# Kernel tuning notes

Measured on AMD Instinct MI355X. Metric: run time of the kernel, lower is better.

Reference implementation:

```python
import jax, jax.numpy as jnp
import numpy as np

B, N, H, NHEADS, N_COE, N_SCALES, THRE = 8, 1024, 128, 4, 50, 4, 5.0


def _layernorm(x, g, b, eps=1e-5):
    mu = x.mean(-1, keepdims=True)
    var = ((x - mu) ** 2).mean(-1, keepdims=True)
    return (x - mu) / jnp.sqrt(var + eps) * g + b


def setup_inputs() -> dict:
    key = jax.random.key(0)
    ks = jax.random.split(key, 12)

    def lin(k, out_d, in_d):
        lim = 1.0 / np.sqrt(in_d)
        kw, kb = jax.random.split(k)
        W = jax.random.uniform(kw, (out_d, in_d), minval=-lim, maxval=lim, dtype=jnp.float32)
        b = jax.random.uniform(kb, (out_d,), minval=-lim, maxval=lim, dtype=jnp.float32)
        return W, b

    eigw_W, eigw_b = lin(ks[0], H, H + 1)
    qkv_W, qkv_b = lin(ks[1], 3 * H, H)
    out_W, out_b = lin(ks[2], H, H)
    ffn1_W, ffn1_b = lin(ks[3], H, H)
    ffn2_W, ffn2_b = lin(ks[4], H, H)
    dsc_W, dsc_b = lin(ks[5], N_COE, H)
    dwav_W, dwav_b = lin(ks[6], N_COE, H)
    dscl_W, dscl_b = lin(ks[7], N_SCALES, H)
    # normalized-Laplacian eigenvalues live in [0, 2]
    eigenvalue = jax.random.uniform(ks[8], (B, N), minval=0.0, maxval=2.0, dtype=jnp.float32)
    eigenvector = jax.random.normal(ks[9], (B, N, N), dtype=jnp.float32) / np.sqrt(N)
    length = jnp.full((B,), N, dtype=jnp.int32)  # full graphs -> static shapes under jit
    return dict(
        eigenvalue=eigenvalue, eigenvector=eigenvector,
        eigw_W=eigw_W, eigw_b=eigw_b,
        ln1_g=jnp.ones((H,), jnp.float32), ln1_b=jnp.zeros((H,), jnp.float32),
        qkv_W=qkv_W, qkv_b=qkv_b, out_W=out_W, out_b=out_b,
        ln2_g=jnp.ones((H,), jnp.float32), ln2_b=jnp.zeros((H,), jnp.float32),
        ffn1_W=ffn1_W, ffn1_b=ffn1_b, ffn2_W=ffn2_W, ffn2_b=ffn2_b,
        dsc_W=dsc_W, dsc_b=dsc_b, dwav_W=dwav_W, dwav_b=dwav_b,
        dscl_W=dscl_W, dscl_b=dscl_b, length=length)


def _forward(eigenvalue, eigenvector, eigw_W, eigw_b, ln1_g, ln1_b, qkv_W, qkv_b,
             out_W, out_b, ln2_g, ln2_b, ffn1_W, ffn1_b, ffn2_W, ffn2_b,
             dsc_W, dsc_b, dwav_W, dwav_b, dscl_W, dscl_b, length):
    Bn, Nn = eigenvalue.shape
    mask1d = jnp.arange(Nn)[None, :] >= length[:, None]  # [B,N] True = padding

    # ---- SineEncoding ----
    ee = eigenvalue * 100.0
    div = jnp.exp(jnp.arange(0, H, 2, dtype=jnp.float32) * (-np.log(10000.0) / H))
    pe = ee[:, :, None] * div  # [B,N,H/2]
    eeig = jnp.concatenate([eigenvalue[:, :, None], jnp.sin(pe), jnp.cos(pe)], -1)  # [B,N,H+1]
    eig = eeig @ eigw_W.T + eigw_b  # [B,N,H]

    # ---- MHA block (pre-norm, residual) ----
    x = _layernorm(eig, ln1_g, ln1_b)
    qkv = x @ qkv_W.T + qkv_b
    q, k, v = jnp.split(qkv, 3, axis=-1)
    dh = H // NHEADS
    heads = lambda t: t.reshape(Bn, Nn, NHEADS, dh).transpose(0, 2, 1, 3)
    q, k, v = heads(q), heads(k), heads(v)
    scores = jnp.einsum('bhnd,bhmd->bhnm', q, k) / np.sqrt(dh)
    scores = jnp.where(mask1d[:, None, None, :], -1e9, scores)
    attn = jax.nn.softmax(scores, axis=-1)
    o = jnp.einsum('bhnm,bhmd->bhnd', attn, v).transpose(0, 2, 1, 3).reshape(Bn, Nn, H)
    eig = eig + (o @ out_W.T + out_b)

    # ---- FFN block (pre-norm, residual) ----
    y = _layernorm(eig, ln2_g, ln2_b)
    y = jax.nn.gelu(y @ ffn1_W.T + ffn1_b, approximate=False) @ ffn2_W.T + ffn2_b
    eig = eig + y

    # ---- decoders: masked mean-pool over eigenvalue axis ----
    len_f = length.astype(eig.dtype)[:, None] + 1e-8

    def pooled(W, b):
        c = eig @ W.T + b
        c = jnp.where(mask1d[:, :, None], 0.0, c)
        return c.sum(1) / len_f

    coe_scaling = jax.nn.sigmoid(pooled(dsc_W, dsc_b))          # [B,n_coe]
    coe_scaling = coe_scaling / (coe_scaling.sum(-1, keepdims=True) + 1e-8)
    coe_wavelet = jax.nn.sigmoid(pooled(dwav_W, dwav_b))        # [B,n_coe]
    coe_wavelet = coe_wavelet / (coe_wavelet.sum(-1, keepdims=True) + 1e-8)
    coe_scales = jax.nn.sigmoid(pooled(dscl_W, dscl_b)) * THRE  # [B,n_scales]

    # ---- Chebyshev-like recurrence (gen_base) via scan ----
    def gen_base(yv):
        te0, to0 = jnp.ones_like(yv), yv
        def step(carry, _):
            te, to = carry
            te = 2.0 * yv * to - te
            to = 2.0 * yv * te - to
            return (te, to), (te, to)
        _, (evens, odds) = jax.lax.scan(step, (te0, to0), None, length=N_COE - 1)
        wav = jnp.concatenate([te0[None], evens], 0)   # [n_coe, ...]
        scal = jnp.concatenate([to0[None], odds], 0)
        return scal, wav

    base_scaling, _ = gen_base(eigenvalue[:, :, None] - 1.0)  # [n_coe,B,N,1]
    fsw = eigenvalue[:, :, None] * coe_scales[:, None, :]     # [B,N,S]
    fsw = jnp.where(fsw > 2.0, 0.0, fsw)
    _, base_wavelet = gen_base(fsw - 1.0)                     # [n_coe,B,N,S]
    base_scaling = 0.5 * (1.0 - base_scaling)
    base_wavelet = 0.5 * (1.0 - base_wavelet)

    curr_scaling = jnp.einsum('bc,cbns->bns', coe_scaling, base_scaling)  # [B,N,1]
    curr_wavelet = jnp.einsum('bc,cbns->bns', coe_wavelet, base_wavelet)  # [B,N,S]
    fsa = jnp.concatenate([curr_scaling, curr_wavelet], -1)               # [B,N,S+1]
    # tight-frame normalization (cfg.lam.tight_use = True)
    fsa = fsa / (jnp.linalg.norm(fsa, axis=-1, keepdims=True) + 1e-8)

    # filters_i = evc @ diag(fsa[:,:,i]) @ evc^T, all scales at once
    filters = jnp.einsum('bnk,bks,bmk->bsnm', eigenvector, fsa, eigenvector)
    # F.normalize(filters) with default dim=1 -> normalize over row axis (n here)
    norm = jnp.sqrt(jnp.sum(filters ** 2, axis=2, keepdims=True))
    filters = filters / jnp.maximum(norm, 1e-12)
    # filters[edge_idx] with full lengths == flatten over (B,N,N), per scale
    bases = filters.transpose(1, 0, 2, 3).reshape(N_SCALES + 1, -1)
    return bases


def reference(eigenvalue, eigenvector, eigw_W, eigw_b, ln1_g, ln1_b, qkv_W, qkv_b,
              out_W, out_b, ln2_g, ln2_b, ffn1_W, ffn1_b, ffn2_W, ffn2_b,
              dsc_W, dsc_b, dwav_W, dwav_b, dscl_W, dscl_b, length):
    return _forward(eigenvalue, eigenvector, eigw_W, eigw_b, ln1_g, ln1_b, qkv_W, qkv_b,
                    out_W, out_b, ln2_g, ln2_b, ffn1_W, ffn1_b, ffn2_W, ffn2_b,
                    dsc_W, dsc_b, dwav_W, dwav_b, dscl_W, dscl_b, length)
```

## Files before the change

kernel.cpp:

```cpp
#include <hip/hip_runtime.h>
#include <hip/hip_bf16.h>
#include <cstdint>

#define BB 8
#define NV 1024
#define HH 128
#define DH 32
#define NCOE 50
#define NSC 4

#define WOFF_EIG 0
#define WOFF_QKV 16384
#define WOFF_OUT 65536
#define WOFF_F1  81920
#define WOFF_F2  98304
#define WB_ELEMS 114688

typedef __attribute__((ext_vector_type(8))) short short8;
typedef __attribute__((ext_vector_type(4))) float f32x4;

__device__ __forceinline__ ushort f2bf(float f) {
    uint32_t x = __float_as_uint(f);
    uint32_t r = x + 0x7FFFu + ((x >> 16) & 1u);
    return (ushort)(r >> 16);
}

#define GLDS(gp, lp) __builtin_amdgcn_global_load_lds((const __attribute__((address_space(1))) void*)(gp), (__attribute__((address_space(3))) void*)(lp), 16, 0, 0)

__global__ void k_wcvt(const float* __restrict__ eigw_W, const float* __restrict__ qkv_W,
                       const float* __restrict__ out_W, const float* __restrict__ f1W,
                       const float* __restrict__ f2W, ushort* __restrict__ Wb) {
    int idx = blockIdx.x * 256 + threadIdx.x;
    float v; int dst;
    if (idx < 16384) {
        int r = idx >> 7, k = idx & 127;
        v = eigw_W[r * 129 + 1 + k];
        dst = WOFF_EIG + (k >> 5) * 4096 + r * 32 + (k & 31);
    } else if (idx < 65536) {
        int l = idx - 16384; int c = l >> 14, rem = l & 16383;
        int r = rem >> 7, k = rem & 127;
        v = qkv_W[(size_t)(c * 128 + r) * 128 + k];
        dst = WOFF_QKV + c * 16384 + (k >> 5) * 4096 + r * 32 + (k & 31);
    } else if (idx < 81920) {
        int l = idx - 65536; int r = l >> 7, k = l & 127;
        v = out_W[r * 128 + k];
        dst = WOFF_OUT + (k >> 5) * 4096 + r * 32 + (k & 31);
    } else if (idx < 98304) {
        int l = idx - 81920; int r = l >> 7, k = l & 127;
        v = f1W[r * 128 + k];
        dst = WOFF_F1 + (k >> 5) * 4096 + r * 32 + (k & 31);
    } else {
        int l = idx - 98304; int r = l >> 7, k = l & 127;
        v = f2W[r * 128 + k];
        dst = WOFF_F2 + (k >> 5) * 4096 + r * 32 + (k & 31);
    }
    Wb[dst] = f2bf(v);
}

__global__ __launch_bounds__(256) void k_enc_sine(const float* __restrict__ ev, const ushort* __restrict__ Wb,
                                                  const float* __restrict__ eigw_W, const float* __restrict__ eigw_b,
                                                  float* __restrict__ eig) {
    __shared__ ushort As[16384];
    __shared__ ushort Bs[16384];
    int row0 = blockIdx.x * 128;
    int t = threadIdx.x, lane = t & 63, w = t >> 6;
    int wr = w >> 1, wc = w & 1;
#pragma unroll
    for (int p = 0; p < 8; ++p) {
        int ci = w * 8 + p;
        GLDS(Wb + WOFF_EIG + ci * 512 + lane * 8, Bs + ci * 512);
    }
    {
        int r = t >> 1, half = t & 1;
        float e = ev[row0 + r] * 100.0f;
#pragma unroll
        for (int ch = 0; ch < 8; ++ch) {
            short8 u;
#pragma unroll
            for (int l = 0; l < 8; ++l) {
                int j = ch * 8 + l;
                float div = expf((float)(2 * j) * -0.07195578415606394f);
                float pe = e * div;
                u[l] = (short)f2bf(half ? cosf(pe) : sinf(pe));
            }
            int k = half * 64 + ch * 8;
            *(short8*)(As + (k >> 5) * 4096 + r * 32 + (k & 31)) = u;
        }
    }
    __syncthreads();
    int cl = lane & 15, q = lane >> 4;
    f32x4 acc[4][4] = {};
#pragma unroll
    for (int kt = 0; kt < 4; ++kt) {
        const ushort* ap = As + kt * 4096 + (wr * 64 + cl) * 32 + q * 8;
        const ushort* bp = Bs + kt * 4096 + (wc * 64 + cl) * 32 + q * 8;
        short8 af[4], bfr[4];
#pragma unroll
        for (int i = 0; i < 4; ++i) af[i] = *(const short8*)(ap + i * 512);
#pragma unroll
        for (int j = 0; j < 4; ++j) bfr[j] = *(const short8*)(bp + j * 512);
#pragma unroll
        for (int i = 0; i < 4; ++i)
#pragma unroll
            for (int j = 0; j < 4; ++j)
                acc[i][j] = __builtin_amdgcn_mfma_f32_16x16x32_bf16(af[i], bfr[j], acc[i][j], 0, 0, 0);
    }
#pragma unroll
    for (int i = 0; i < 4; ++i) {
        int rbase = wr * 64 + i * 16 + q * 4;
        float er[4];
#pragma unroll
        for (int r = 0; r < 4; ++r) er[r] = ev[row0 + rbase + r];
#pragma unroll
        for (int j = 0; j < 4; ++j) {
            int col = wc * 64 + j * 16 + cl;
            float w0 = eigw_W[col * 129];
            float bv = eigw_b[col];
#pragma unroll
            for (int r = 0; r < 4; ++r)
                eig[(size_t)(row0 + rbase + r) * HH + col] = acc[i][j][r] + er[r] * w0 + bv;
        }
    }
}

__global__ __launch_bounds__(256) void k_enc_qkv(const float* __restrict__ eig, const float* __restrict__ g,
                                                 const float* __restrict__ be, const ushort* __restrict__ Wb,
                                                 const float* __restrict__ bias,
                                                 ushort* __restrict__ qb, ushort* __restrict__ kb, ushort* __restrict__ vb) {
    __shared__ ushort As[16384];
    __shared__ ushort Bs[16384];
    int row0 = blockIdx.x * 128;
    int t = threadIdx.x, lane = t & 63, w = t >> 6;
    int wr = w >> 1, wc = w & 1;
    {
        int r = t >> 1, half = t & 1;
        const float4* rowp = (const float4*)(eig + (size_t)(row0 + r) * HH + half * 64);
        float4 v[16];
        float s = 0.f, s2 = 0.f;
#pragma unroll
        for (int i = 0; i < 16; ++i) {
            float4 a = rowp[i]; v[i] = a;
            s += a.x + a.y + a.z + a.w;
            s2 += a.x * a.x + a.y * a.y + a.z * a.z + a.w * a.w;
        }
        s += __shfl_xor(s, 1); s2 += __shfl_xor(s2, 1);
        float mean = s * 0.0078125f;
        float var = s2 * 0.0078125f - mean * mean;
        float rstd = rsqrtf(var + 1e-5f);
        const float4* g4 = (const float4*)(g + half * 64);
        const float4* b4 = (const float4*)(be + half * 64);
#pragma unroll
        for (int ch = 0; ch < 8; ++ch) {
            float4 a = v[2 * ch], b2 = v[2 * ch + 1];
            float4 ga = g4[2 * ch], gb = g4[2 * ch + 1];
            float4 ba = b4[2 * ch], bb = b4[2 * ch + 1];
            short8 u;
            u[0] = (short)f2bf((a.x - mean) * rstd * ga.x + ba.x);
            u[1] = (short)f2bf((a.y - mean) * rstd * ga.y + ba.y);
            u[2] = (short)f2bf((a.z - mean) * rstd * ga.z + ba.z);
            u[3] = (short)f2bf((a.w - mean) * rstd * ga.w + ba.w);
            u[4] = (short)f2bf((b2.x - mean) * rstd * gb.x + bb.x);
            u[5] = (short)f2bf((b2.y - mean) * rstd * gb.y + bb.y);
            u[6] = (short)f2bf((b2.z - mean) * rstd * gb.z + bb.z);
            u[7] = (short)f2bf((b2.w - mean) * rstd * gb.w + bb.w);
            int k = half * 64 + ch * 8;
            *(short8*)(As + (k >> 5) * 4096 + r * 32 + (k & 31)) = u;
        }
    }
    int cl = lane & 15, q = lane >> 4;
    int bidx = row0 >> 10, nbase = row0 & (NV - 1);
    ushort* dsts[3] = {qb, kb, vb};
#pragma unroll 1
    for (int c = 0; c < 3; ++c) {
        __syncthreads();
#pragma unroll
        for (int p = 0; p < 8; ++p) {
            int ci = w * 8 + p;
            GLDS(Wb + WOFF_QKV + c * 16384 + ci * 512 + lane * 8, Bs + ci * 512);
        }
        __syncthreads();
        f32x4 acc[4][4] = {};
#pragma unroll
        for (int kt = 0; kt < 4; ++kt) {
            const ushort* ap = As + kt * 4096 + (wr * 64 + cl) * 32 + q * 8;
            const ushort* bp = Bs + kt * 4096 + (wc * 64 + cl) * 32 + q * 8;
            short8 af[4], bfr[4];
#pragma unroll
            for (int i = 0; i < 4; ++i) af[i] = *(const short8*)(ap + i * 512);
#pragma unroll
            for (int j = 0; j < 4; ++j) bfr[j] = *(const short8*)(bp + j * 512);
#pragma unroll
            for (int i = 0; i < 4; ++i)
#pragma unroll
                for (int j = 0; j < 4; ++j)
                    acc[i][j] = __builtin_amdgcn_mfma_f32_16x16x32_bf16(af[i], bfr[j], acc[i][j], 0, 0, 0);
        }
        ushort* dst = dsts[c];
#pragma unroll
        for (int j = 0; j < 4; ++j) {
            int col = wc * 64 + j * 16 + cl;
            float bv = bias[c * 128 + col];
            int h = col >> 5, dd = col & 31;
            ushort* hb = dst + ((size_t)(bidx * 4 + h) * NV + nbase) * DH + dd;
#pragma unroll
            for (int i = 0; i < 4; ++i) {
                int rbase = wr * 64 + i * 16 + q * 4;
#pragma unroll
                for (int r = 0; r < 4; ++r)
                    hb[(size_t)(rbase + r) * DH] = f2bf(acc[i][j][r] + bv);
            }
        }
    }
}

__global__ __launch_bounds__(256) void k_vt(const ushort* __restrict__ vb, ushort* __restrict__ vt) {
    __shared__ ushort Ld[256 * 40];
    int bh = blockIdx.y, n0 = blockIdx.x * 256;
    int t = threadIdx.x;
    const ushort* src = vb + ((size_t)bh * NV + n0) * DH;
#pragma unroll
    for (int p = 0; p < 4; ++p) {
        int idx = p * 256 + t;
        int rowi = idx >> 2, ch = idx & 3;
        short8 u = *(const short8*)(src + idx * 8);
        *(short8*)(&Ld[rowi * 40 + ch * 8]) = u;
    }
    __syncthreads();
    int d = t >> 3, nc = (t & 7) * 32;
    ushort* dst = vt + ((size_t)bh * DH + d) * NV + n0 + nc;
#pragma unroll
    for (int p = 0; p < 4; ++p) {
        short8 u;
#pragma unroll
        for (int i = 0; i < 8; ++i) u[i] = (short)Ld[(nc + p * 8 + i) * 40 + d];
        *(short8*)(dst + p * 8) = u;
    }
}

__global__ __launch_bounds__(256) void k_qk(const ushort* __restrict__ qb, const ushort* __restrict__ kb,
                                            float* __restrict__ S) {
    __shared__ ushort As[128 * 32];
    __shared__ ushort Bs[128 * 32];
    int tile = blockIdx.x;
    int bh = blockIdx.y;
    int n0 = (tile >> 3) * 128, m0 = (tile & 7) * 128;
    int tid = threadIdx.x, lane = tid & 63, w = tid >> 6;
    int wr = w >> 1, wc = w & 1;
    const ushort* qt = qb + ((size_t)bh * NV + n0) * DH;
    const ushort* ktb = kb + ((size_t)bh * NV + m0) * DH;
#pragma unroll
    for (int p = 0; p < 2; ++p) {
        int ci = w * 2 + p;
        GLDS(qt + ci * 512 + lane * 8, As + ci * 512);
        GLDS(ktb + ci * 512 + lane * 8, Bs + ci * 512);
    }
    __syncthreads();
    int cl = lane & 15, q = lane >> 4;
    const ushort* ap = As + ((wr * 64 + cl) * 32 + q * 8);
    const ushort* bp = Bs + ((wc * 64 + cl) * 32 + q * 8);
    short8 af[4], bfr[4];
#pragma unroll
    for (int i = 0; i < 4; ++i) af[i] = *(const short8*)(ap + i * 512);
#pragma unroll
    for (int j = 0; j < 4; ++j) bfr[j] = *(const short8*)(bp + j * 512);
    f32x4 acc[4][4] = {};
#pragma unroll
    for (int i = 0; i < 4; ++i)
#pragma unroll
        for (int j = 0; j < 4; ++j)
            acc[i][j] = __builtin_amdgcn_mfma_f32_16x16x32_bf16(af[i], bfr[j], acc[i][j], 0, 0, 0);
    size_t sb = (size_t)bh * NV * NV;
#pragma unroll
    for (int i = 0; i < 4; ++i) {
        int rbase = n0 + wr * 64 + i * 16 + q * 4;
#pragma unroll
        for (int j = 0; j < 4; ++j) {
            int col = m0 + wc * 64 + j * 16 + cl;
#pragma unroll
            for (int r = 0; r < 4; ++r)
                S[sb + (size_t)(rbase + r) * NV + col] = acc[i][j][r] * 0.17677669529663687f;
        }
    }
}

__global__ __launch_bounds__(256) void k_softmax(float* __restrict__ S) {
    __shared__ float red[4];
    int row = blockIdx.x, t = threadIdx.x, lane = t & 63;
    float* rp = S + (size_t)row * NV;
    float4 v = ((const float4*)rp)[t];
    float m = fmaxf(fmaxf(v.x, v.y), fmaxf(v.z, v.w));
#pragma unroll
    for (int off = 32; off; off >>= 1) m = fmaxf(m, __shfl_xor(m, off));
    if (lane == 0) red[t >> 6] = m;
    __syncthreads();
    m = fmaxf(fmaxf(red[0], red[1]), fmaxf(red[2], red[3]));
    __syncthreads();
    float e0 = __expf(v.x - m), e1 = __expf(v.y - m), e2 = __expf(v.z - m), e3 = __expf(v.w - m);
    float s4 = e0 + e1 + e2 + e3;
#pragma unroll
    for (int off = 32; off; off >>= 1) s4 += __shfl_xor(s4, off);
    if (lane == 0) red[t >> 6] = s4;
    __syncthreads();
    float inv = 1.0f / (red[0] + red[1] + red[2] + red[3]);
    ushort4 o;
    o.x = f2bf(e0 * inv); o.y = f2bf(e1 * inv); o.z = f2bf(e2 * inv); o.w = f2bf(e3 * inv);
    ((ushort4*)rp)[t] = o;
}

__global__ __launch_bounds__(256) void k_pv(const float* __restrict__ Sf, const ushort* __restrict__ vt,
                                            ushort* __restrict__ obuf) {
    __shared__ ushort As[128 * 32];
    __shared__ ushort Bs[32 * 32];
    int n0 = blockIdx.x * 128, bh = blockIdx.y;
    int b = bh >> 2, h = bh & 3;
    int tid = threadIdx.x, lane = tid & 63, w = tid >> 6;
    const char* Sb = (const char*)Sf;
    const ushort* vtb = vt + (size_t)bh * DH * NV;
    f32x4 acc[2][2] = {};
    for (int kt = 0; kt < NV / 32; ++kt) {
        int k0 = kt * 32;
        __syncthreads();
#pragma unroll
        for (int p = 0; p < 2; ++p) {
            int ci = w * 2 + p;
            int rrow = ci * 16 + (lane >> 2);
            int kch = (lane & 3) * 8;
            const ushort* gp = (const ushort*)(Sb + (size_t)(bh * NV + n0 + rrow) * 4096) + k0 + kch;
            GLDS(gp, As + ci * 512);
        }
        if (tid < 128) {
            int d = tid >> 2, ch = tid & 3;
            short8 u = *(const short8*)(vtb + (size_t)d * NV + k0 + ch * 8);
            *(short8*)(&Bs[d * 32 + ch * 8]) = u;
        }
        __syncthreads();
        int cl = lane & 15, q = lane >> 4;
        const ushort* ap = As + ((w * 32 + cl) * 32 + q * 8);
        const ushort* bp = Bs + (cl * 32 + q * 8);
        short8 af[2], bfr[2];
#pragma unroll
        for (int i = 0; i < 2; ++i) af[i] = *(const short8*)(ap + i * 512);
#pragma unroll
        for (int j = 0; j < 2; ++j) bfr[j] = *(const short8*)(bp + j * 512);
#pragma unroll
        for (int i = 0; i < 2; ++i)
#pragma unroll
            for (int j = 0; j < 2; ++j)
                acc[i][j] = __builtin_amdgcn_mfma_f32_16x16x32_bf16(af[i], bfr[j], acc[i][j], 0, 0, 0);
    }
    int cl = lane & 15, q = lane >> 4;
#pragma unroll
    for (int i = 0; i < 2; ++i) {
        int rbase = n0 + w * 32 + i * 16 + q * 4;
#pragma unroll
        for (int j = 0; j < 2; ++j) {
            int d = j * 16 + cl;
#pragma unroll
            for (int r = 0; r < 4; ++r)
                obuf[((size_t)(b * NV + rbase + r)) * HH + h * DH + d] = f2bf(acc[i][j][r]);
        }
    }
}

__global__ __launch_bounds__(256) void k_enc_proj(const ushort* __restrict__ obuf, const ushort* __restrict__ Wb,
                                                  const float* __restrict__ bias, float* __restrict__ eig) {
    __shared__ ushort As[16384];
    __shared__ ushort Bs[16384];
    int row0 = blockIdx.x * 128;
    int t = threadIdx.x, lane = t & 63, w = t >> 6;
    int wr = w >> 1, wc = w & 1;
#pragma unroll
    for (int p = 0; p < 8; ++p) {
        int ci = w * 8 + p;
        int kt = ci >> 3, rb = ci & 7;
        const ushort* gp = obuf + (size_t)(row0 + rb * 16 + (lane >> 2)) * HH + kt * 32 + (lane & 3) * 8;
        GLDS(gp, As + kt * 4096 + rb * 512);
        GLDS(Wb + WOFF_OUT + ci * 512 + lane * 8, Bs + ci * 512);
    }
    __syncthreads();
    int cl = lane & 15, q = lane >> 4;
    f32x4 acc[4][4] = {};
#pragma unroll
    for (int kt = 0; kt < 4; ++kt) {
        const ushort* ap = As + kt * 4096 + (wr * 64 + cl) * 32 + q * 8;
        const ushort* bp = Bs + kt * 4096 + (wc * 64 + cl) * 32 + q * 8;
        short8 af[4], bfr[4];
#pragma unroll
        for (int i = 0; i < 4; ++i) af[i] = *(const short8*)(ap + i * 512);
#pragma unroll
        for (int j = 0; j < 4; ++j) bfr[j] = *(const short8*)(bp + j * 512);
#pragma unroll
        for (int i = 0; i < 4; ++i)
#pragma unroll
            for (int j = 0; j < 4; ++j)
                acc[i][j] = __builtin_amdgcn_mfma_f32_16x16x32_bf16(af[i], bfr[j], acc[i][j], 0, 0, 0);
    }
#pragma unroll
    for (int j = 0; j < 4; ++j) {
        int col = wc * 64 + j * 16 + cl;
        float bv = bias[col];
#pragma unroll
        for (int i = 0; i < 4; ++i) {
            int rbase = wr * 64 + i * 16 + q * 4;
#pragma unroll
            for (int r = 0; r < 4; ++r) {
                size_t o = (size_t)(row0 + rbase + r) * HH + col;
                eig[o] += acc[i][j][r] + bv;
            }
        }
    }
}

__global__ __launch_bounds__(256) void k_enc_ffn(float* __restrict__ eig, const float* __restrict__ g,
                                                 const float* __restrict__ be, const ushort* __restrict__ Wb,
                                                 const float* __restrict__ b1, const float* __restrict__ b2) {
    __shared__ ushort As[16384];
    __shared__ ushort Bs[16384];
    int row0 = blockIdx.x * 128;
    int t = threadIdx.x, lane = t & 63, w = t >> 6;
    int wr = w >> 1, wc = w & 1;
    {
        int r = t >> 1, half = t & 1;
        const float4* rowp = (const float4*)(eig + (size_t)(row0 + r) * HH + half * 64);
        float4 v[16];
        float s = 0.f, s2 = 0.f;
#pragma unroll
        for (int i = 0; i < 16; ++i) {
            float4 a = rowp[i]; v[i] = a;
            s += a.x + a.y + a.z + a.w;
            s2 += a.x * a.x + a.y * a.y + a.z * a.z + a.w * a.w;
        }
        s += __shfl_xor(s, 1); s2 += __shfl_xor(s2, 1);
        float mean = s * 0.0078125f;
        float var = s2 * 0.0078125f - mean * mean;
        float rstd = rsqrtf(var + 1e-5f);
        const float4* g4 = (const float4*)(g + half * 64);
        const float4* b4 = (const float4*)(be + half * 64);
#pragma unroll
        for (int ch = 0; ch < 8; ++ch) {
            float4 a = v[2 * ch], bq = v[2 * ch + 1];
            float4 ga = g4[2 * ch], gb = g4[2 * ch + 1];
            float4 ba = b4[2 * ch], bb = b4[2 * ch + 1];
            short8 u;
            u[0] = (short)f2bf((a.x - mean) * rstd * ga.x + ba.x);
            u[1] = (short)f2bf((a.y - mean) * rstd * ga.y + ba.y);
            u[2] = (short)f2bf((a.z - mean) * rstd * ga.z + ba.z);
            u[3] = (short)f2bf((a.w - mean) * rstd * ga.w + ba.w);
            u[4] = (short)f2bf((bq.x - mean) * rstd * gb.x + bb.x);
            u[5] = (short)f2bf((bq.y - mean) * rstd * gb.y + bb.y);
            u[6] = (short)f2bf((bq.z - mean) * rstd * gb.z + bb.z);
            u[7] = (short)f2bf((bq.w - mean) * rstd * gb.w + bb.w);
            int k = half * 64 + ch * 8;
            *(short8*)(As + (k >> 5) * 4096 + r * 32 + (k & 31)) = u;
        }
    }
#pragma unroll
    for (int p = 0; p < 8; ++p) {
        int ci = w * 8 + p;
        GLDS(Wb + WOFF_F1 + ci * 512 + lane * 8, Bs + ci * 512);
    }
    __syncthreads();
    int cl = lane & 15, q = lane >> 4;
    f32x4 acc[4][4] = {};
#pragma unroll
    for (int kt = 0; kt < 4; ++kt) {
        const ushort* ap = As + kt * 4096 + (wr * 64 + cl) * 32 + q * 8;
        const ushort* bp = Bs + kt * 4096 + (wc * 64 + cl) * 32 + q * 8;
        short8 af[4], bfr[4];
#pragma unroll
        for (int i = 0; i < 4; ++i) af[i] = *(const short8*)(ap + i * 512);
#pragma unroll
        for (int j = 0; j < 4; ++j) bfr[j] = *(const short8*)(bp + j * 512);
#pragma unroll
        for (int i = 0; i < 4; ++i)
#pragma unroll
            for (int j = 0; j < 4; ++j)
                acc[i][j] = __builtin_amdgcn_mfma_f32_16x16x32_bf16(af[i], bfr[j], acc[i][j], 0, 0, 0);
    }
    __syncthreads();
#pragma unroll
    for (int j = 0; j < 4; ++j) {
        int col = wc * 64 + j * 16 + cl;
        float bv = b1[col];
        int koff = (col >> 5) * 4096 + (col & 31);
#pragma unroll
        for (int i = 0; i < 4; ++i) {
            int rbase = wr * 64 + i * 16 + q * 4;
#pragma unroll
            for (int r = 0; r < 4; ++r) {
                float a = acc[i][j][r] + bv;
                float ge = 0.5f * a * (1.0f + erff(a * 0.7071067811865475f));
                As[koff + (rbase + r) * 32] = f2bf(ge);
            }
        }
    }
#pragma unroll
    for (int p = 0; p < 8; ++p) {
        int ci = w * 8 + p;
        GLDS(Wb + WOFF_F2 + ci * 512 + lane * 8, Bs + ci * 512);
    }
    __syncthreads();
    f32x4 acc2[4][4] = {};
#pragma unroll
    for (int kt = 0; kt < 4; ++kt) {
        const ushort* ap = As + kt * 4096 + (wr * 64 + cl) * 32 + q * 8;
        const ushort* bp = Bs + kt * 4096 + (wc * 64 + cl) * 32 + q * 8;
        short8 af[4], bfr[4];
#pragma unroll
        for (int i = 0; i < 4; ++i) af[i] = *(const short8*)(ap + i * 512);
#pragma unroll
        for (int j = 0; j < 4; ++j) bfr[j] = *(const short8*)(bp + j * 512);
#pragma unroll
        for (int i = 0; i < 4; ++i)
#pragma unroll
            for (int j = 0; j < 4; ++j)
                acc2[i][j] = __builtin_amdgcn_mfma_f32_16x16x32_bf16(af[i], bfr[j], acc2[i][j], 0, 0, 0);
    }
#pragma unroll
    for (int j = 0; j < 4; ++j) {
        int col = wc * 64 + j * 16 + cl;
        float bv = b2[col];
#pragma unroll
        for (int i = 0; i < 4; ++i) {
            int rbase = wr * 64 + i * 16 + q * 4;
#pragma unroll
            for (int r = 0; r < 4; ++r) {
                size_t o = (size_t)(row0 + rbase + r) * HH + col;
                eig[o] += acc2[i][j][r] + bv;
            }
        }
    }
}

__global__ __launch_bounds__(1024) void k_meanpool(const float* __restrict__ eig, float* __restrict__ me) {
    __shared__ float part[8][HH];
    int b = blockIdx.x, t = threadIdx.x;
    int col = t & 127, grp = t >> 7;
    const float* p = eig + (size_t)b * NV * HH + (size_t)grp * 128 * HH + col;
    float s = 0.f;
    for (int n = 0; n < 128; ++n) s += p[(size_t)n * HH];
    part[grp][col] = s;
    __syncthreads();
    if (t < 128) {
        float a = 0.f;
#pragma unroll
        for (int g2 = 0; g2 < 8; ++g2) a += part[g2][t];
        me[b * HH + t] = a * (1.0f / NV);
    }
}

__global__ void k_decoders(const float* __restrict__ me,
                           const float* __restrict__ dscW, const float* __restrict__ dscb,
                           const float* __restrict__ dwavW, const float* __restrict__ dwavb,
                           const float* __restrict__ dsclW, const float* __restrict__ dsclb,
                           float* __restrict__ cs, float* __restrict__ cw, float* __restrict__ csc) {
    __shared__ float m[HH];
    __shared__ float s1[NCOE], s2[NCOE];
    __shared__ float sums[2];
    int b = blockIdx.x, t = threadIdx.x;
    m[t] = me[b * HH + t];
    m[t + 64] = me[b * HH + t + 64];
    __syncthreads();
    if (t < NCOE) {
        float a = dscb[t], a2 = dwavb[t];
        const float* w1 = dscW + t * HH;
        const float* w2 = dwavW + t * HH;
        for (int j = 0; j < HH; ++j) { a += m[j] * w1[j]; a2 += m[j] * w2[j]; }
        s1[t] = 1.f / (1.f + __expf(-a));
        s2[t] = 1.f / (1.f + __expf(-a2));
    }
    if (t < NSC) {
        float a = dsclb[t];
        const float* wv = dsclW + t * HH;
        for (int j = 0; j < HH; ++j) a += m[j] * wv[j];
        csc[b * NSC + t] = 5.0f / (1.f + __expf(-a));
    }
    __syncthreads();
    if (t == 0) {
        float a = 0.f, bb = 0.f;
        for (int c = 0; c < NCOE; ++c) { a += s1[c]; bb += s2[c]; }
        sums[0] = a; sums[1] = bb;
    }
    __syncthreads();
    if (t < NCOE) {
        cs[b * NCOE + t] = s1[t] / (sums[0] + 1e-8f);
        cw[b * NCOE + t] = s2[t] / (sums[1] + 1e-8f);
    }
}

__global__ void k_fsa(const float* __restrict__ ev, const float* __restrict__ cs,
                      const float* __restrict__ cw, const float* __restrict__ csc,
                      float* __restrict__ fsaT, float* __restrict__ fsqT) {
    __shared__ float lcs[NCOE], lcw[NCOE], lsc[NSC];
    int gid = blockIdx.x * 256 + threadIdx.x;
    int b = gid >> 10, n = gid & (NV - 1);
    int t = threadIdx.x;
    if (t < NCOE) { lcs[t] = cs[b * NCOE + t]; lcw[t] = cw[b * NCOE + t]; }
    if (t < NSC) lsc[t] = csc[b * NSC + t];
    __syncthreads();
    float e = ev[gid];
    float x = e - 1.0f;
    float te = 1.f, to = x;
    float a0 = lcs[0] * 0.5f * (1.f - to);
    for (int c = 1; c < NCOE; ++c) {
        te = 2.f * x * to - te;
        to = 2.f * x * te - to;
        a0 += lcs[c] * 0.5f * (1.f - to);
    }
    float aw[NSC];
#pragma unroll
    for (int s = 0; s < NSC; ++s) {
        float f = e * lsc[s];
        if (f > 2.0f) f = 0.0f;
        float y = f - 1.0f;
        float te2 = 1.f, to2 = y, a = 0.f;
        for (int c = 1; c < NCOE; ++c) {
            te2 = 2.f * y * to2 - te2;
            to2 = 2.f * y * te2 - to2;
            a += lcw[c] * 0.5f * (1.f - te2);
        }
        aw[s] = a;
    }
    float n2 = a0 * a0;
#pragma unroll
    for (int s = 0; s < NSC; ++s) n2 += aw[s] * aw[s];
    float inv = 1.f / (sqrtf(n2) + 1e-8f);
    float v0 = a0 * inv;
    fsaT[((size_t)b * 5 + 0) * NV + n] = v0;
    if (fsqT) fsqT[((size_t)b * 5 + 0) * NV + n] = sqrtf(fmaxf(v0, 0.f));
#pragma unroll
    for (int s = 0; s < NSC; ++s) {
        float vs = aw[s] * inv;
        fsaT[((size_t)b * 5 + 1 + s) * NV + n] = vs;
        if (fsqT) fsqT[((size_t)b * 5 + 1 + s) * NV + n] = sqrtf(fmaxf(vs, 0.f));
    }
}

__global__ void k_tobf16(const float* __restrict__ in, ushort* __restrict__ outp) {
    int i = blockIdx.x * 256 + threadIdx.x;
    const float4* p = (const float4*)in + (size_t)i * 2;
    float4 a = p[0], bq = p[1];
    uint4 r;
    r.x = (uint)f2bf(a.x) | ((uint)f2bf(a.y) << 16);
    r.y = (uint)f2bf(a.z) | ((uint)f2bf(a.w) << 16);
    r.z = (uint)f2bf(bq.x) | ((uint)f2bf(bq.y) << 16);
    r.w = (uint)f2bf(bq.z) | ((uint)f2bf(bq.w) << 16);
    ((uint4*)outp)[i] = r;
}

__global__ __launch_bounds__(256) void k_prescale(const float* __restrict__ evec, const float* __restrict__ fsq,
                                                  ushort* __restrict__ Asc) {
    int gid = blockIdx.x * 256 + threadIdx.x;
    int gk = gid & 127;
    int n = (gid >> 7) & (NV - 1);
    int b = gid >> 17;
    const float4* vp = (const float4*)(evec + ((size_t)b * NV + n) * NV + gk * 8);
    float4 a = vp[0], c = vp[1];
    int gsw = (gk & ~3) | ((gk ^ (n >> 2)) & 3);
    size_t dstbase = ((size_t)(b * 5) * NV + n) * NV + (size_t)gsw * 8;
#pragma unroll
    for (int s = 0; s < 5; ++s) {
        const float* fp = fsq + (size_t)(b * 5 + s) * NV + gk * 8;
        float4 f0 = *(const float4*)fp, f1 = *(const float4*)(fp + 4);
        uint4 r;
        r.x = (uint)f2bf(a.x * f0.x) | ((uint)f2bf(a.y * f0.y) << 16);
        r.y = (uint)f2bf(a.z * f0.z) | ((uint)f2bf(a.w * f0.w) << 16);
        r.z = (uint)f2bf(c.x * f1.x) | ((uint)f2bf(c.y * f1.y) << 16);
        r.w = (uint)f2bf(c.z * f1.z) | ((uint)f2bf(c.w * f1.w) << 16);
        *(uint4*)(Asc + dstbase + (size_t)s * NV * NV) = r;
    }
}

__global__ __launch_bounds__(256) void k_gemm_sym(const ushort* __restrict__ Asc,
                                                  float* __restrict__ out,
                                                  float* __restrict__ cn) {
    __shared__ ushort As[2][4096];
    __shared__ ushort Bs[2][4096];
    int lin = blockIdx.x;
    int wg = (lin & 7) * 180 + (lin >> 3);
    int bs = wg / 36, p = wg % 36;
    int b = bs / 5, s = bs % 5;
    int ti = 0, rem = p;
    while (rem >= 8 - ti) { rem -= 8 - ti; ++ti; }
    int tj = ti + rem;
    int n0 = ti * 128, m0 = tj * 128;
    int tid = threadIdx.x, lane = tid & 63, w = tid >> 6;
    int wr = w >> 1, wc = w & 1;
    const ushort* Abase = Asc + (size_t)(b * 5 + s) * NV * NV;
    const ushort* an = Abase + (size_t)n0 * NV;
    const ushort* am = Abase + (size_t)m0 * NV;
    int rrow0 = lane >> 2;
    int kch = (lane & 3) * 8;
    int cl = lane & 15, q = lane >> 4;
    int qx = (q ^ (cl >> 2)) & 3;
    int fo = cl * 32 + qx * 8;

    auto STAGE = [&](int nb, int k0) {
#pragma unroll
        for (int p2 = 0; p2 < 2; ++p2) {
            int ci = w * 2 + p2;
            int rr = ci * 16 + rrow0;
            GLDS(an + (size_t)rr * NV + k0 + kch, &As[nb][ci * 512]);
            GLDS(am + (size_t)rr * NV + k0 + kch, &Bs[nb][ci * 512]);
        }
    };

    f32x4 acc[4][4] = {};
    STAGE(0, 0);
    __syncthreads();
    for (int kt = 0; kt < 31; ++kt) {
        int cur = kt & 1;
        STAGE(cur ^ 1, (kt + 1) * 32);
        short8 af[4], bfr[4];
#pragma unroll
        for (int i = 0; i < 4; ++i) af[i] = *(const short8*)(&As[cur][(wr * 4 + i) * 512 + fo]);
#pragma unroll
        for (int j = 0; j < 4; ++j) bfr[j] = *(const short8*)(&Bs[cur][(wc * 4 + j) * 512 + fo]);
#pragma unroll
        for (int i = 0; i < 4; ++i)
#pragma unroll
            for (int j = 0; j < 4; ++j)
                acc[i][j] = __builtin_amdgcn_mfma_f32_16x16x32_bf16(af[i], bfr[j], acc[i][j], 0, 0, 0);
        __syncthreads();
    }
    {
        short8 af[4], bfr[4];
#pragma unroll
        for (int i = 0; i < 4; ++i) af[i] = *(const short8*)(&As[1][(wr * 4 + i) * 512 + fo]);
#pragma unroll
        for (int j = 0; j < 4; ++j) bfr[j] = *(const short8*)(&Bs[1][(wc * 4 + j) * 512 + fo]);
#pragma unroll
        for (int i = 0; i < 4; ++i)
#pragma unroll
            for (int j = 0; j < 4; ++j)
                acc[i][j] = __builtin_amdgcn_mfma_f32_16x16x32_bf16(af[i], bfr[j], acc[i][j], 0, 0, 0);
    }
    size_t ob = (size_t)(s * BB + b) * NV * NV;
    float* cnb = cn + (size_t)(s * BB + b) * NV;
    float colss[4] = {0.f, 0.f, 0.f, 0.f};
    float rowss[4][4];
#pragma unroll
    for (int i = 0; i < 4; ++i)
#pragma unroll
        for (int r = 0; r < 4; ++r) rowss[i][r] = 0.f;
#pragma unroll
    for (int i = 0; i < 4; ++i) {
        int rbase = n0 + wr * 64 + i * 16 + q * 4;
#pragma unroll
        for (int j = 0; j < 4; ++j) {
            int col = m0 + wc * 64 + j * 16 + cl;
#pragma unroll
            for (int r = 0; r < 4; ++r) {
                float v = acc[i][j][r];
                out[ob + (size_t)(rbase + r) * NV + col] = v;
                colss[j] += v * v;
                rowss[i][r] += v * v;
            }
        }
    }
#pragma unroll
    for (int j = 0; j < 4; ++j) {
        float v = colss[j];
        v += __shfl_xor(v, 16);
        v += __shfl_xor(v, 32);
        if (q == 0) atomicAdd(cnb + (m0 + wc * 64 + j * 16 + cl), v);
    }
    if (ti != tj) {
#pragma unroll
        for (int i = 0; i < 4; ++i)
#pragma unroll
            for (int r = 0; r < 4; ++r) {
                float v = rowss[i][r];
                v += __shfl_xor(v, 1); v += __shfl_xor(v, 2);
                v += __shfl_xor(v, 4); v += __shfl_xor(v, 8);
                if (cl == 0) atomicAdd(cnb + (n0 + wr * 64 + i * 16 + q * 4 + r), v);
            }
    }
}

__global__ __launch_bounds__(256) void k_gemm(const ushort* __restrict__ Vb,
                                              const float* __restrict__ fsaT,
                                              float* __restrict__ out,
                                              float* __restrict__ cn) {
    __shared__ ushort As[128 * 32];
    __shared__ ushort Bs[128 * 32];
    int tile = blockIdx.x;
    int bsid = blockIdx.y;
    int b = bsid / 5, s = bsid % 5;
    int n0 = (tile >> 3) * 128, m0 = (tile & 7) * 128;
    int tid = threadIdx.x, lane = tid & 63, w = tid >> 6;
    int wr = w >> 1, wc = w & 1;
    const ushort* Vbase = Vb + (size_t)b * NV * NV;
    const float* fs = fsaT + ((size_t)b * 5 + s) * NV;
    f32x4 acc[4][4] = {};

    for (int kt = 0; kt < NV / 32; ++kt) {
        int k0 = kt * 32;
        __syncthreads();
#pragma unroll
        for (int p = 0; p < 2; ++p) {
            int ci = w * 2 + p;
            int rrow = ci * 16 + (lane >> 2);
            int kch = (lane & 3) * 8;
            const ushort* gp = Vbase + (size_t)(m0 + rrow) * NV + k0 + kch;
            GLDS(gp, Bs + ci * 512);
        }
#pragma unroll
        for (int p = 0; p < 2; ++p) {
            int idx = p * 256 + tid;
            int rrow = idx >> 2;
            int kch = (idx & 3) * 8;
            const ushort* gp = Vbase + (size_t)(n0 + rrow) * NV + k0 + kch;
            uint4 raw = *(const uint4*)gp;
            const float4* fp = (const float4*)(fs + k0 + kch);
            float4 f0 = fp[0], f1 = fp[1];
            float v0 = __uint_as_float(raw.x << 16) * f0.x;
            float v1 = __uint_as_float(raw.x & 0xffff0000u) * f0.y;
            float v2 = __uint_as_float(raw.y << 16) * f0.z;
            float v3 = __uint_as_float(raw.y & 0xffff0000u) * f0.w;
            float v4 = __uint_as_float(raw.z << 16) * f1.x;
            float v5 = __uint_as_float(raw.z & 0xffff0000u) * f1.y;
            float v6 = __uint_as_float(raw.w << 16) * f1.z;
            float v7 = __uint_as_float(raw.w & 0xffff0000u) * f1.w;
            uint4 rr;
            rr.x = (uint)f2bf(v0) | ((uint)f2bf(v1) << 16);
            rr.y = (uint)f2bf(v2) | ((uint)f2bf(v3) << 16);
            rr.z = (uint)f2bf(v4) | ((uint)f2bf(v5) << 16);
            rr.w = (uint)f2bf(v6) | ((uint)f2bf(v7) << 16);
            *(uint4*)(As + rrow * 32 + kch) = rr;
        }
        __syncthreads();
        int cl = lane & 15, q = lane >> 4;
        const ushort* ap = As + ((wr * 64 + cl) * 32 + q * 8);
        const ushort* bp = Bs + ((wc * 64 + cl) * 32 + q * 8);
        short8 af[4], bfr[4];
#pragma unroll
        for (int i = 0; i < 4; ++i) af[i] = *(const short8*)(ap + i * 512);
#pragma unroll
        for (int j = 0; j < 4; ++j) bfr[j] = *(const short8*)(bp + j * 512);
#pragma unroll
        for (int i = 0; i < 4; ++i)
#pragma unroll
            for (int j = 0; j < 4; ++j)
                acc[i][j] = __builtin_amdgcn_mfma_f32_16x16x32_bf16(af[i], bfr[j], acc[i][j], 0, 0, 0);
    }
    int cl = lane & 15, q = lane >> 4;
    size_t ob = (size_t)(s * BB + b) * NV * NV;
    float colss[4] = {0.f, 0.f, 0.f, 0.f};
#pragma unroll
    for (int i = 0; i < 4; ++i) {
        int rbase = n0 + wr * 64 + i * 16 + q * 4;
#pragma unroll
        for (int j = 0; j < 4; ++j) {
            int col = m0 + wc * 64 + j * 16 + cl;
#pragma unroll
            for (int r = 0; r < 4; ++r) {
                float v = acc[i][j][r];
                out[ob + (size_t)(rbase + r) * NV + col] = v;
                colss[j] += v * v;
            }
        }
    }
    float* cnb = cn + (size_t)(s * BB + b) * NV;
#pragma unroll
    for (int j = 0; j < 4; ++j) {
        float v = colss[j];
        v += __shfl_xor(v, 16);
        v += __shfl_xor(v, 32);
        if (q == 0) atomicAdd(cnb + (m0 + wc * 64 + j * 16 + cl), v);
    }
}

__global__ __launch_bounds__(256) void k_norm_sym(float* __restrict__ out, const float* __restrict__ cn) {
    __shared__ float L[128][68];
    int ti = blockIdx.x >> 3, tj = blockIdx.x & 7;
    if (ti > tj) return;
    int bs = blockIdx.y;
    int n0 = ti * 128, m0 = tj * 128;
    size_t ob = (size_t)bs * NV * NV;
    const float* cnb = cn + (size_t)bs * NV;
    int t = threadIdx.x;
#pragma unroll 1
    for (int ch = 0; ch < 2; ++ch) {
        if (ch) __syncthreads();
#pragma unroll
        for (int p = 0; p < 8; ++p) {
            int idx = p * 256 + t;
            int r = idx >> 5;
            int c4 = (idx & 31) * 4;
            size_t o = ob + (size_t)(n0 + ch * 64 + r) * NV + m0 + c4;
            float4 v = *(float4*)(out + o);
            float4 sm = *(const float4*)(cnb + m0 + c4);
            float4 wv;
            wv.x = v.x * (1.f / fmaxf(sqrtf(sm.x), 1e-12f));
            wv.y = v.y * (1.f / fmaxf(sqrtf(sm.y), 1e-12f));
            wv.z = v.z * (1.f / fmaxf(sqrtf(sm.z), 1e-12f));
            wv.w = v.w * (1.f / fmaxf(sqrtf(sm.w), 1e-12f));
            *(float4*)(out + o) = wv;
            if (ti != tj) {
                L[c4 + 0][r] = v.x; L[c4 + 1][r] = v.y;
                L[c4 + 2][r] = v.z; L[c4 + 3][r] = v.w;
            }
        }
        if (ti != tj) {
            __syncthreads();
#pragma unroll
            for (int p = 0; p < 8; ++p) {
                int idx = p * 256 + t;
                int mr = idx >> 4;
                int j4 = (idx & 15) * 4;
                float4 sn = *(const float4*)(cnb + n0 + ch * 64 + j4);
                float4 wv;
                wv.x = L[mr][j4 + 0] * (1.f / fmaxf(sqrtf(sn.x), 1e-12f));
                wv.y = L[mr][j4 + 1] * (1.f / fmaxf(sqrtf(sn.y), 1e-12f));
                wv.z = L[mr][j4 + 2] * (1.f / fmaxf(sqrtf(sn.z), 1e-12f));
                wv.w = L[mr][j4 + 3] * (1.f / fmaxf(sqrtf(sn.w), 1e-12f));
                *(float4*)(out + ob + (size_t)(m0 + mr) * NV + n0 + ch * 64 + j4) = wv;
            }
        }
    }
}

__global__ void k_norm(float* __restrict__ out, const float* __restrict__ cn) {
    int bid = blockIdx.x;
    int bs = bid >> 10, n = bid & (NV - 1);
    int m4 = threadIdx.x * 4;
    float4 ssv = *(const float4*)(cn + (size_t)bs * NV + m4);
    float4* p = (float4*)(out + ((size_t)bs * NV + n) * NV + m4);
    float4 v = *p;
    v.x *= 1.f / fmaxf(sqrtf(ssv.x), 1e-12f);
    v.y *= 1.f / fmaxf(sqrtf(ssv.y), 1e-12f);
    v.z *= 1.f / fmaxf(sqrtf(ssv.z), 1e-12f);
    v.w *= 1.f / fmaxf(sqrtf(ssv.w), 1e-12f);
    *p = v;
}

extern "C" void kernel_launch(void* const* d_in, const int* in_sizes, int n_in,
                              void* d_out, int out_size, void* d_ws, size_t ws_size,
                              hipStream_t stream) {
    const float* eigenvalue = (const float*)d_in[0];
    const float* eigenvector = (const float*)d_in[1];
    const float* eigw_W = (const float*)d_in[2];
    const float* eigw_b = (const float*)d_in[3];
    const float* ln1_g = (const float*)d_in[4];
    const float* ln1_b = (const float*)d_in[5];
    const float* qkv_W = (const float*)d_in[6];
    const float* qkv_b = (const float*)d_in[7];
    const float* out_W = (const float*)d_in[8];
    const float* out_b = (const float*)d_in[9];
    const float* ln2_g = (const float*)d_in[10];
    const float* ln2_b = (const float*)d_in[11];
    const float* ffn1_W = (const float*)d_in[12];
    const float* ffn1_b = (const float*)d_in[13];
    const float* ffn2_W = (const float*)d_in[14];
    const float* ffn2_b = (const float*)d_in[15];
    const float* dsc_W = (const float*)d_in[16];
    const float* dsc_b = (const float*)d_in[17];
    const float* dwav_W = (const float*)d_in[18];
    const float* dwav_b = (const float*)d_in[19];
    const float* dscl_W = (const float*)d_in[20];
    const float* dscl_b = (const float*)d_in[21];

    char* w = (char*)d_ws;
    float* eig  = (float*)(w + 0);
    float* me   = (float*)(w + 4194304);
    float* cs   = (float*)(w + 4198400);
    float* cw   = (float*)(w + 4200448);
    float* csc  = (float*)(w + 4202496);
    float* fsaT = (float*)(w + 4203520);
    float* cn   = (float*)(w + 4367360);
    ushort* qb  = (ushort*)(w + 4531200);
    ushort* kb  = (ushort*)(w + 6628352);
    ushort* vb  = (ushort*)(w + 8725504);
    ushort* vt  = (ushort*)(w + 10822656);
    ushort* obuf = (ushort*)(w + 12919808);
    ushort* Wb  = (ushort*)(w + 15016960);
    ushort* Vb  = (ushort*)(w + 15246336);

    bool big = ws_size >= (size_t)117440512;
    float* fsqT = big ? (float*)(w + 32023552) : nullptr;
    ushort* Asc = (ushort*)(w + 33554432);

    float* outp = (float*)d_out;
    float* S = (float*)d_out;

    hipMemsetAsync(cn, 0, 40 * NV * sizeof(float), stream);

    k_wcvt<<<dim3(WB_ELEMS / 256), dim3(256), 0, stream>>>(eigw_W, qkv_W, out_W, ffn1_W, ffn2_W, Wb);
    k_enc_sine<<<dim3(64), dim3(256), 0, stream>>>(eigenvalue, Wb, eigw_W, eigw_b, eig);
    k_enc_qkv<<<dim3(64), dim3(256), 0, stream>>>(eig, ln1_g, ln1_b, Wb, qkv_b, qb, kb, vb);
    k_vt<<<dim3(4, 32), dim3(256), 0, stream>>>(vb, vt);
    k_qk<<<dim3(64, 32), dim3(256), 0, stream>>>(qb, kb, S);
    k_softmax<<<dim3(32 * NV), dim3(256), 0, stream>>>(S);
    k_pv<<<dim3(8, 32), dim3(256), 0, stream>>>(S, vt, obuf);
    k_enc_proj<<<dim3(64), dim3(256), 0, stream>>>(obuf, Wb, out_b, eig);
    k_enc_ffn<<<dim3(64), dim3(256), 0, stream>>>(eig, ln2_g, ln2_b, Wb, ffn1_b, ffn2_b);
    k_meanpool<<<dim3(BB), dim3(1024), 0, stream>>>(eig, me);
    k_decoders<<<dim3(BB), dim3(64), 0, stream>>>(me, dsc_W, dsc_b, dwav_W, dwav_b, dscl_W, dscl_b, cs, cw, csc);
    k_fsa<<<dim3(BB * NV / 256), dim3(256), 0, stream>>>(eigenvalue, cs, cw, csc, fsaT, fsqT);
    if (big) {
        k_prescale<<<dim3(BB * NV * 128 / 256), dim3(256), 0, stream>>>(eigenvector, fsqT, Asc);
        k_gemm_sym<<<dim3(36 * 40), dim3(256), 0, stream>>>(Asc, outp, cn);
        k_norm_sym<<<dim3(64, 40), dim3(256), 0, stream>>>(outp, cn);
    } else {
        k_tobf16<<<dim3(BB * NV * NV / (8 * 256)), dim3(256), 0, stream>>>(eigenvector, Vb);
        k_gemm<<<dim3(64, 40), dim3(256), 0, stream>>>(Vb, fsaT, outp, cn);
        k_norm<<<dim3(40 * NV), dim3(256), 0, stream>>>(outp, cn);
    }
}
```

Baseline: 525.9 us.

## Fuse QK, softmax and PV into a flash-attention style kernel

Replaces the three-kernel attention (materialize the scaled score matrix in fp32, row softmax in place writing bf16, then a PV GEMM) with one kernel using online softmax. Each wave handles 16 query rows, computes scores per 128-key block with MFMA, keeps a running max and sum, stages bf16 probabilities in per-wave LDS, and accumulates P·V in registers. This removes the roughly 128 MB score-matrix write and reread plus two launches. In exchange K and V are read straight from global memory with no LDS sharing across waves, and only 512 blocks are launched.

```diff
diff --git a/kernel.cpp b/kernel.cpp
--- a/kernel.cpp
+++ b/kernel.cpp
@@ -237,128 +237,79 @@
     }
 }
 
-__global__ __launch_bounds__(256) void k_qk(const ushort* __restrict__ qb, const ushort* __restrict__ kb,
-                                            float* __restrict__ S) {
-    __shared__ ushort As[128 * 32];
-    __shared__ ushort Bs[128 * 32];
-    int tile = blockIdx.x;
-    int bh = blockIdx.y;
-    int n0 = (tile >> 3) * 128, m0 = (tile & 7) * 128;
-    int tid = threadIdx.x, lane = tid & 63, w = tid >> 6;
-    int wr = w >> 1, wc = w & 1;
-    const ushort* qt = qb + ((size_t)bh * NV + n0) * DH;
-    const ushort* ktb = kb + ((size_t)bh * NV + m0) * DH;
-#pragma unroll
-    for (int p = 0; p < 2; ++p) {
-        int ci = w * 2 + p;
-        GLDS(qt + ci * 512 + lane * 8, As + ci * 512);
-        GLDS(ktb + ci * 512 + lane * 8, Bs + ci * 512);
-    }
-    __syncthreads();
+__global__ __launch_bounds__(256) void k_attn(const ushort* __restrict__ qb, const ushort* __restrict__ kb,
+                                              const ushort* __restrict__ vt, ushort* __restrict__ obuf) {
+    __shared__ ushort Ps[4][16][136];
+    int n0 = blockIdx.x * 64, bh = blockIdx.y;
+    int b = bh >> 2, h = bh & 3;
+    int t = threadIdx.x, lane = t & 63, w = t >> 6;
     int cl = lane & 15, q = lane >> 4;
-    const ushort* ap = As + ((wr * 64 + cl) * 32 + q * 8);
-    const ushort* bp = Bs + ((wc * 64 + cl) * 32 + q * 8);
-    short8 af[4], bfr[4];
-#pragma unroll
-    for (int i = 0; i < 4; ++i) af[i] = *(const short8*)(ap + i * 512);
-#pragma unroll
-    for (int j = 0; j < 4; ++j) bfr[j] = *(const short8*)(bp + j * 512);
-    f32x4 acc[4][4] = {};
-#pragma unroll
-    for (int i = 0; i < 4; ++i)
-#pragma unroll
-        for (int j = 0; j < 4; ++j)
-            acc[i][j] = __builtin_amdgcn_mfma_f32_16x16x32_bf16(af[i], bfr[j], acc[i][j], 0, 0, 0);
-    size_t sb = (size_t)bh * NV * NV;
-#pragma unroll
-    for (int i = 0; i < 4; ++i) {
-        int rbase = n0 + wr * 64 + i * 16 + q * 4;
-#pragma unroll
-        for (int j = 0; j < 4; ++j) {
-            int col = m0 + wc * 64 + j * 16 + cl;
+    short8 qf = *(const short8*)(qb + ((size_t)bh * NV + n0 + w * 16 + cl) * DH + q * 8);
+    const ushort* kbase = kb + (size_t)bh * NV * DH;
+    const ushort* vbase = vt + (size_t)bh * DH * NV;
+    ushort (*P)[136] = Ps[w];
+    const float scale = 0.17677669529663687f;
+    float m[4], l[4];
+#pragma unroll
+    for (int r = 0; r < 4; ++r) { m[r] = -1e30f; l[r] = 0.f; }
+    f32x4 oacc[2] = {};
+#pragma unroll 1
+    for (int kt = 0; kt < 8; ++kt) {
+        f32x4 acc[8] = {};
+#pragma unroll
+        for (int j = 0; j < 8; ++j) {
+            short8 kf = *(const short8*)(kbase + (size_t)(kt * 128 + j * 16 + cl) * DH + q * 8);
+            acc[j] = __builtin_amdgcn_mfma_f32_16x16x32_bf16(qf, kf, acc[j], 0, 0, 0);
+        }
+#pragma unroll
+        for (int r = 0; r < 4; ++r) {
+            float rm = -1e30f;
+#pragma unroll
+            for (int j = 0; j < 8; ++j) rm = fmaxf(rm, acc[j][r]);
+            rm = fmaxf(rm, __shfl_xor(rm, 1));
+            rm = fmaxf(rm, __shfl_xor(rm, 2));
+            rm = fmaxf(rm, __shfl_xor(rm, 4));
+            rm = fmaxf(rm, __shfl_xor(rm, 8));
+            rm *= scale;
+            float mn = fmaxf(m[r], rm);
+            float corr = __expf(m[r] - mn);
+            float ps = 0.f;
+#pragma unroll
+            for (int j = 0; j < 8; ++j) {
+                float p = __expf(acc[j][r] * scale - mn);
+                acc[j][r] = p;
+                ps += p;
+            }
+            ps += __shfl_xor(ps, 1); ps += __shfl_xor(ps, 2);
+            ps += __shfl_xor(ps, 4); ps += __shfl_xor(ps, 8);
+            l[r] = l[r] * corr + ps;
+            m[r] = mn;
+            oacc[0][r] *= corr;
+            oacc[1][r] *= corr;
+        }
+#pragma unroll
+        for (int j = 0; j < 8; ++j)
 #pragma unroll
             for (int r = 0; r < 4; ++r)
-                S[sb + (size_t)(rbase + r) * NV + col] = acc[i][j][r] * 0.17677669529663687f;
-        }
-    }
-}
-
-__global__ __launch_bounds__(256) void k_softmax(float* __restrict__ S) {
-    __shared__ float red[4];
-    int row = blockIdx.x, t = threadIdx.x, lane = t & 63;
-    float* rp = S + (size_t)row * NV;
-    float4 v = ((const float4*)rp)[t];
-    float m = fmaxf(fmaxf(v.x, v.y), fmaxf(v.z, v.w));
-#pragma unroll
-    for (int off = 32; off; off >>= 1) m = fmaxf(m, __shfl_xor(m, off));
-    if (lane == 0) red[t >> 6] = m;
-    __syncthreads();
-    m = fmaxf(fmaxf(red[0], red[1]), fmaxf(red[2], red[3]));
-    __syncthreads();
-    float e0 = __expf(v.x - m), e1 = __expf(v.y - m), e2 = __expf(v.z - m), e3 = __expf(v.w - m);
-    float s4 = e0 + e1 + e2 + e3;
-#pragma unroll
-    for (int off = 32; off; off >>= 1) s4 += __shfl_xor(s4, off);
-    if (lane == 0) red[t >> 6] = s4;
-    __syncthreads();
-    float inv = 1.0f / (red[0] + red[1] + red[2] + red[3]);
-    ushort4 o;
-    o.x = f2bf(e0 * inv); o.y = f2bf(e1 * inv); o.z = f2bf(e2 * inv); o.w = f2bf(e3 * inv);
-    ((ushort4*)rp)[t] = o;
-}
-
-__global__ __launch_bounds__(256) void k_pv(const float* __restrict__ Sf, const ushort* __restrict__ vt,
-                                            ushort* __restrict__ obuf) {
-    __shared__ ushort As[128 * 32];
-    __shared__ ushort Bs[32 * 32];
-    int n0 = blockIdx.x * 128, bh = blockIdx.y;
-    int b = bh >> 2, h = bh & 3;
-    int tid = threadIdx.x, lane = tid & 63, w = tid >> 6;
-    const char* Sb = (const char*)Sf;
-    const ushort* vtb = vt + (size_t)bh * DH * NV;
-    f32x4 acc[2][2] = {};
-    for (int kt = 0; kt < NV / 32; ++kt) {
-        int k0 = kt * 32;
-        __syncthreads();
-#pragma unroll
-        for (int p = 0; p < 2; ++p) {
-            int ci = w * 2 + p;
-            int rrow = ci * 16 + (lane >> 2);
-            int kch = (lane & 3) * 8;
-            const ushort* gp = (const ushort*)(Sb + (size_t)(bh * NV + n0 + rrow) * 4096) + k0 + kch;
-            GLDS(gp, As + ci * 512);
-        }
-        if (tid < 128) {
-            int d = tid >> 2, ch = tid & 3;
-            short8 u = *(const short8*)(vtb + (size_t)d * NV + k0 + ch * 8);
-            *(short8*)(&Bs[d * 32 + ch * 8]) = u;
-        }
-        __syncthreads();
-        int cl = lane & 15, q = lane >> 4;
-        const ushort* ap = As + ((w * 32 + cl) * 32 + q * 8);
-        const ushort* bp = Bs + (cl * 32 + q * 8);
-        short8 af[2], bfr[2];
-#pragma unroll
-        for (int i = 0; i < 2; ++i) af[i] = *(const short8*)(ap + i * 512);
-#pragma unroll
-        for (int j = 0; j < 2; ++j) bfr[j] = *(const short8*)(bp + j * 512);
-#pragma unroll
-        for (int i = 0; i < 2; ++i)
-#pragma unroll
-            for (int j = 0; j < 2; ++j)
-                acc[i][j] = __builtin_amdgcn_mfma_f32_16x16x32_bf16(af[i], bfr[j], acc[i][j], 0, 0, 0);
-    }
-    int cl = lane & 15, q = lane >> 4;
-#pragma unroll
-    for (int i = 0; i < 2; ++i) {
-        int rbase = n0 + w * 32 + i * 16 + q * 4;
-#pragma unroll
-        for (int j = 0; j < 2; ++j) {
-            int d = j * 16 + cl;
-#pragma unroll
-            for (int r = 0; r < 4; ++r)
-                obuf[((size_t)(b * NV + rbase + r)) * HH + h * DH + d] = f2bf(acc[i][j][r]);
-        }
+                P[q * 4 + r][j * 16 + cl] = f2bf(acc[j][r]);
+#pragma unroll
+        for (int ks = 0; ks < 4; ++ks) {
+            short8 pf = *(const short8*)(&P[cl][ks * 32 + q * 8]);
+#pragma unroll
+            for (int j2 = 0; j2 < 2; ++j2) {
+                short8 vf = *(const short8*)(vbase + (size_t)(j2 * 16 + cl) * NV + kt * 128 + ks * 32 + q * 8);
+                oacc[j2] = __builtin_amdgcn_mfma_f32_16x16x32_bf16(pf, vf, oacc[j2], 0, 0, 0);
+            }
+        }
+    }
+#pragma unroll
+    for (int r = 0; r < 4; ++r) {
+        float inv = 1.0f / l[r];
+        int row = n0 + w * 16 + q * 4 + r;
+        ushort* orow = obuf + ((size_t)(b * NV + row)) * HH + h * DH;
+#pragma unroll
+        for (int j2 = 0; j2 < 2; ++j2)
+            orow[j2 * 16 + cl] = f2bf(oacc[j2][r] * inv);
     }
 }
 
@@ -982,7 +933,6 @@
     ushort* Asc = (ushort*)(w + 33554432);
 
     float* outp = (float*)d_out;
-    float* S = (float*)d_out;
 
     hipMemsetAsync(cn, 0, 40 * NV * sizeof(float), stream);
 
@@ -990,9 +940,7 @@
     k_enc_sine<<<dim3(64), dim3(256), 0, stream>>>(eigenvalue, Wb, eigw_W, eigw_b, eig);
     k_enc_qkv<<<dim3(64), dim3(256), 0, stream>>>(eig, ln1_g, ln1_b, Wb, qkv_b, qb, kb, vb);
     k_vt<<<dim3(4, 32), dim3(256), 0, stream>>>(vb, vt);
-    k_qk<<<dim3(64, 32), dim3(256), 0, stream>>>(qb, kb, S);
-    k_softmax<<<dim3(32 * NV), dim3(256), 0, stream>>>(S);
-    k_pv<<<dim3(8, 32), dim3(256), 0, stream>>>(S, vt, obuf);
+    k_attn<<<dim3(16, 32), dim3(256), 0, stream>>>(qb, kb, vt, obuf);
     k_enc_proj<<<dim3(64), dim3(256), 0, stream>>>(obuf, Wb, out_b, eig);
     k_enc_ffn<<<dim3(64), dim3(256), 0, stream>>>(eig, ln2_g, ln2_b, Wb, ffn1_b, ffn2_b);
     k_meanpool<<<dim3(BB), dim3(1024), 0, stream>>>(eig, me);
```

New measurement: 489.8 us. 1.07x faster.
